# Performance work log

Hardware: AMD Instinct MI355X
Metric: run time of the kernel (lower is better)

## Reference

```python
import jax, jax.numpy as jnp
import numpy as np

OS_FACTOR = 1.5

def setup_inputs() -> dict:
    key = jax.random.key(0)
    k = jax.random.split(key, 5)
    B, T, I, H = 64, 1024, 1024, 1024
    s = 1.0 / np.sqrt(H).astype(np.float32)
    return {
        "x": jax.random.normal(k[0], (B, T, I), dtype=jnp.float32),
        "W_ih": jax.random.normal(k[1], (H, I), dtype=jnp.float32) * s,
        "W_hh": jax.random.normal(k[2], (H, H), dtype=jnp.float32) * s,
        "b_ih": jax.random.normal(k[3], (H,), dtype=jnp.float32) * s,
        "b_hh": jax.random.normal(k[4], (H,), dtype=jnp.float32) * s,
    }

def reference(x, W_ih, W_hh, b_ih, b_hh):
    B, T, I = x.shape
    H = W_hh.shape[0]
    delay_near = int(np.floor(OS_FACTOR))   # 1
    delay_far = int(np.ceil(OS_FACTOR))     # 2
    alpha = jnp.float32(OS_FACTOR - delay_near)  # 0.5
    # Precompute input projection for all steps (same math, batched GEMM): [T,B,H]
    xw = jnp.einsum('bti,hi->tbh', x, W_ih) + b_ih + b_hh
    # Circular delay buffer of the last `delay_far` states, zero-initialized.
    # In the torch code, negative indices into the zero `states` buffer read zeros,
    # which matches a zero-initialized buffer here.
    buf0 = jnp.zeros((delay_far, B, H), dtype=x.dtype)

    def step(buf, xw_t):
        # buf[-1] = state at t-1, buf[0] = state at t-delay_far
        h_read = (1.0 - alpha) * buf[delay_far - delay_near] + alpha * buf[0]
        h = jnp.tanh(xw_t + h_read @ W_hh.T)
        buf = jnp.concatenate([buf[1:], h[None]], axis=0)
        return buf, h

    _, states = jax.lax.scan(step, buf0, xw)   # states: [T,B,H]
    states = jnp.swapaxes(states, 0, 1)        # [B,T,H]
    h_final = states[:, -1, :][None]           # [1,B,H]
    return states, h_final
```

## Files before the change

### kernel.cpp

```cpp
#include <hip/hip_runtime.h>
#include <stdint.h>
#include <stddef.h>

#define TT 1024
#define BB 64
#define HH 1024
#define II 1024

typedef __attribute__((ext_vector_type(8))) short s16x8;
typedef __attribute__((ext_vector_type(4))) float f32x4;
typedef __attribute__((ext_vector_type(2))) unsigned u32x2;

#define WS_FLAGS 512
#define WS_RING  4096

static __device__ __forceinline__ unsigned short f2bf(float f) {
    union { float f; unsigned int u; } v; v.f = f;
    return (unsigned short)((v.u + 0x7fffu + ((v.u >> 16) & 1u)) >> 16);
}

static __device__ __forceinline__ s16x8 pack8(float4 a, float4 b) {
    s16x8 v;
    v[0] = (short)f2bf(a.x); v[1] = (short)f2bf(a.y);
    v[2] = (short)f2bf(a.z); v[3] = (short)f2bf(a.w);
    v[4] = (short)f2bf(b.x); v[5] = (short)f2bf(b.y);
    v[6] = (short)f2bf(b.z); v[7] = (short)f2bf(b.w);
    return v;
}

static __device__ __forceinline__ f32x4 zero4() {
    f32x4 v = {0.f, 0.f, 0.f, 0.f};
    return v;
}

static __device__ __forceinline__ s16x8 ld16_sc01(const void* p) {
    s16x8 v;
    asm volatile("global_load_dwordx4 %0, %1, off sc0 sc1" : "=v"(v) : "v"(p));
    return v;
}
static __device__ __forceinline__ unsigned ld4_sc01_wait(const void* p) {
    unsigned v;
    asm volatile("global_load_dword %0, %1, off sc0 sc1\n\ts_waitcnt vmcnt(0)"
                 : "=v"(v) : "v"(p) : "memory");
    return v;
}
static __device__ __forceinline__ void st8_sc01(void* p, u32x2 v) {
    asm volatile("global_store_dwordx2 %0, %1, off sc0 sc1" :: "v"(p), "v"(v) : "memory");
}
#define WAITV(n) do { asm volatile("s_waitcnt vmcnt(" #n ")" ::: "memory"); \
                      __builtin_amdgcn_sched_barrier(0); } while (0)

__global__ void init_ws(unsigned int* w) {
    for (int i = threadIdx.x; i < 640; i += 256)
        __hip_atomic_store(&w[i], 0u, __ATOMIC_RELAXED, __HIP_MEMORY_SCOPE_AGENT);
}

__global__ __launch_bounds__(256, 3) void xw_gemm(
    const float* __restrict__ X,
    const float* __restrict__ Wih,
    const float* __restrict__ bih,
    const float* __restrict__ bhh,
    float* __restrict__ out)
{
    __shared__ unsigned short As[128 * 64];
    __shared__ unsigned short Bs[128 * 64];

    const int tid  = threadIdx.x;
    const int lane = tid & 63;
    const int wid  = tid >> 6;
    const int bm = blockIdx.x >> 3;
    const int bn = blockIdx.x & 7;
    const size_t m0 = (size_t)bm * 128;
    const int n0 = bn * 128;
    const int wm = (wid >> 1) * 64;
    const int wn = (wid & 1) * 64;

    f32x4 acc[4][4];
#pragma unroll
    for (int i = 0; i < 4; ++i)
#pragma unroll
        for (int jj = 0; jj < 4; ++jj) acc[i][jj] = zero4();

    const int srow  = tid >> 1;
    const int shalf = tid & 1;
    const float* xp = X   + (m0 + srow) * (size_t)II + shalf * 32;
    const float* wp = Wih + (size_t)(n0 + srow) * II + shalf * 32;

    for (int kt = 0; kt < II / 64; ++kt) {
#pragma unroll
        for (int i = 0; i < 4; ++i) {
            float4 a0 = *(const float4*)(xp + i * 8);
            float4 a1 = *(const float4*)(xp + i * 8 + 4);
            float4 b0 = *(const float4*)(wp + i * 8);
            float4 b1 = *(const float4*)(wp + i * 8 + 4);
            const int c = shalf * 4 + i;
            const int cw = (c ^ (srow & 7)) << 3;
            *(s16x8*)&As[srow * 64 + cw] = pack8(a0, a1);
            *(s16x8*)&Bs[srow * 64 + cw] = pack8(b0, b1);
        }
        __syncthreads();

#pragma unroll
        for (int kk = 0; kk < 2; ++kk) {
            s16x8 af[4], bf[4];
            const int cs = kk * 4 + (lane >> 4);
#pragma unroll
            for (int mi = 0; mi < 4; ++mi) {
                const int r = wm + mi * 16 + (lane & 15);
                af[mi] = *(const s16x8*)&As[r * 64 + ((cs ^ (r & 7)) << 3)];
            }
#pragma unroll
            for (int ni = 0; ni < 4; ++ni) {
                const int r = wn + ni * 16 + (lane & 15);
                bf[ni] = *(const s16x8*)&Bs[r * 64 + ((cs ^ (r & 7)) << 3)];
            }
#pragma unroll
            for (int mi = 0; mi < 4; ++mi)
#pragma unroll
                for (int ni = 0; ni < 4; ++ni)
                    acc[mi][ni] = __builtin_amdgcn_mfma_f32_16x16x32_bf16(
                        af[mi], bf[ni], acc[mi][ni], 0, 0, 0);
        }
        __syncthreads();
        xp += 64; wp += 64;
    }

#pragma unroll
    for (int ni = 0; ni < 4; ++ni) {
        const int col = n0 + wn + ni * 16 + (lane & 15);
        const float bias = bih[col] + bhh[col];
#pragma unroll
        for (int mi = 0; mi < 4; ++mi) {
            const size_t row = m0 + wm + mi * 16 + ((lane >> 4) << 2);
#pragma unroll
            for (int r = 0; r < 4; ++r)
                out[(row + r) * (size_t)HH + col] = acc[mi][ni][r] + bias;
        }
    }
}

__global__ __launch_bounds__(256, 1) void rnn_scan(
    const float* __restrict__ Whh,
    float* __restrict__ out,
    void* __restrict__ ws)
{
    __shared__ unsigned short Hl[8 * 1024];

    const int tid  = threadIdx.x;
    const int lane = tid & 63;
    const int wid  = tid >> 6;
    const int g  = blockIdx.x >> 4;
    const int sl = blockIdx.x & 15;

    const int jb = sl * 64 + wid * 16;
    const int kg = lane >> 4;

    s16x8 afr[32];
    {
        const float* wr = Whh + (size_t)(jb + (lane & 15)) * HH + kg * 8;
#pragma unroll
        for (int c = 0; c < 32; ++c) {
            float4 p0 = *(const float4*)(wr + c * 32);
            float4 p1 = *(const float4*)(wr + c * 32 + 4);
            afr[c] = pack8(p0, p1);
        }
    }

    unsigned* fl = (unsigned*)((char*)ws + WS_FLAGS) + g * 64;
    char* rg = (char*)ws + WS_RING + (size_t)g * 32768;

    const int srow = tid >> 5;
    const int sseg = tid & 31;
    const char* sbase0 = rg + srow * 2048 + sseg * 16;
    const char* sbase1 = sbase0 + 16384;

    const int bl   = lane & 15;
    const int blv  = bl & 7;
    const int act  = bl < 8;
    const int b    = g * 8 + blv;
    const int f0   = jb + kg * 4;
    const int hrow = blv;

    float hprev[4];

    {
        const size_t idx = ((size_t)b * TT) * HH + f0;
        float4 xw4 = *(const float4*)(out + idx);
        float4 st;
        st.x = tanhf(xw4.x); st.y = tanhf(xw4.y);
        st.z = tanhf(xw4.z); st.w = tanhf(xw4.w);
        hprev[0] = st.x; hprev[1] = st.y; hprev[2] = st.z; hprev[3] = st.w;
        if (act) {
            *(float4*)(out + idx) = st;
            u32x2 pk;
            pk[0] = (unsigned)f2bf(0.5f * st.x) | ((unsigned)f2bf(0.5f * st.y) << 16);
            pk[1] = (unsigned)f2bf(0.5f * st.z) | ((unsigned)f2bf(0.5f * st.w) << 16);
            st8_sc01(rg + 16384 + blv * 2048 + f0 * 2, pk);
        }
    }
    asm volatile("s_waitcnt vmcnt(0)" ::: "memory");
    __syncthreads();
    if (tid == 0)
        __hip_atomic_store(&fl[sl], 1u, __ATOMIC_RELAXED, __HIP_MEMORY_SCOPE_AGENT);

#pragma unroll 1
    for (int t = 1; t < TT; ++t) {
        const size_t xidx = ((size_t)b * TT + t) * HH + f0;
        float4 xw4 = *(const float4*)(out + xidx);

        {
            const unsigned* myp = fl + (lane & 15);
            for (;;) {
                unsigned v = ld4_sc01_wait(myp);
                if (__all((int)(v >= (unsigned)t))) break;
                __builtin_amdgcn_s_sleep(1);
            }
            asm volatile("" ::: "memory");
            __builtin_amdgcn_sched_barrier(0);
        }

        {
            const char* sp = (t & 1) ? sbase1 : sbase0;
            s16x8 v[4];
#pragma unroll
            for (int i = 0; i < 4; ++i) v[i] = ld16_sc01(sp + i * 512);
#pragma unroll
            for (int i = 0; i < 4; ++i) {
                if (i == 0)      { WAITV(3); }
                else if (i == 1) { WAITV(2); }
                else if (i == 2) { WAITV(1); }
                else             { WAITV(0); }
                const int c = sseg + i * 32;
                *(s16x8*)&Hl[srow * 1024 + ((c ^ (srow & 7)) << 3)] = v[i];
            }
        }
        __syncthreads();

        f32x4 acc[4];
#pragma unroll
        for (int i = 0; i < 4; ++i) acc[i] = zero4();
#pragma unroll
        for (int kb = 0; kb < 4; ++kb) {
            s16x8 h8[8];
#pragma unroll
            for (int ki = 0; ki < 8; ++ki) {
                const int cs = (kb * 8 + ki) * 4 + kg;
                h8[ki] = *(const s16x8*)&Hl[hrow * 1024 + ((cs ^ (hrow & 7)) << 3)];
            }
#pragma unroll
            for (int ki = 0; ki < 8; ++ki)
                acc[ki & 3] = __builtin_amdgcn_mfma_f32_16x16x32_bf16(
                    afr[kb * 8 + ki], h8[ki], acc[ki & 3], 0, 0, 0);
        }
        f32x4 accT = acc[0] + acc[1] + acc[2] + acc[3];

        {
            float hn[4];
#pragma unroll
            for (int r = 0; r < 4; ++r)
                hn[r] = tanhf(accT[r] + ((const float*)&xw4)[r]);
            if (act) {
                float4 st; st.x = hn[0]; st.y = hn[1]; st.z = hn[2]; st.w = hn[3];
                *(float4*)(out + xidx) = st;
                if (t == TT - 1) {
                    *(float4*)(out + (size_t)BB * TT * HH + (size_t)b * HH + f0) = st;
                } else {
                    u32x2 pk;
                    pk[0] = (unsigned)f2bf(0.5f * (hn[0] + hprev[0])) |
                            ((unsigned)f2bf(0.5f * (hn[1] + hprev[1])) << 16);
                    pk[1] = (unsigned)f2bf(0.5f * (hn[2] + hprev[2])) |
                            ((unsigned)f2bf(0.5f * (hn[3] + hprev[3])) << 16);
                    char* rw = rg + (size_t)((t + 1) & 1) * 16384;
                    st8_sc01(rw + blv * 2048 + f0 * 2, pk);
                }
            }
#pragma unroll
            for (int r = 0; r < 4; ++r) hprev[r] = hn[r];
        }
        if (t < TT - 1) {
            asm volatile("s_waitcnt vmcnt(0)" ::: "memory");
            __syncthreads();
            if (tid == 0)
                __hip_atomic_store(&fl[sl], (unsigned)(t + 1),
                                   __ATOMIC_RELAXED, __HIP_MEMORY_SCOPE_AGENT);
        }
    }
}

extern "C" void kernel_launch(void* const* d_in, const int* in_sizes, int n_in,
                              void* d_out, int out_size, void* d_ws, size_t ws_size,
                              hipStream_t stream)
{
    const float* X   = (const float*)d_in[0];
    const float* Wih = (const float*)d_in[1];
    const float* Whh = (const float*)d_in[2];
    const float* bih = (const float*)d_in[3];
    const float* bhh = (const float*)d_in[4];
    float* out = (float*)d_out;

    init_ws<<<dim3(1), dim3(256), 0, stream>>>((unsigned int*)d_ws);
    xw_gemm<<<dim3(4096), dim3(256), 0, stream>>>(X, Wih, bih, bhh, out);
    rnn_scan<<<dim3(128), dim3(256), 0, stream>>>(Whh, out, d_ws);
}
```

Baseline: 3.600 ms.

## Halve scan workgroups, widen to 512 threads, and move state stores off the flag path

The recurrent scan now runs 8 workgroups of 512 threads per batch group instead of 16 of 256, so each step waits on half as many cross-workgroup flags. Each wave polls a single flag without sleeping, and the shared-state staging load is remapped to two 16-byte loads per thread. The fp32 state store to the output is moved after the flag publish so it leaves the critical path. The input-projection GEMM also gets a swizzled block order for better cache locality. The cost is more register pressure per workgroup and busier spin-polling.

After: 3.988 ms. 1.11x slower.

```diff
diff --git a/kernel.cpp b/kernel.cpp
--- a/kernel.cpp
+++ b/kernel.cpp
@@ -68,8 +68,9 @@
     const int tid  = threadIdx.x;
     const int lane = tid & 63;
     const int wid  = tid >> 6;
-    const int bm = blockIdx.x >> 3;
-    const int bn = blockIdx.x & 7;
+    const int L  = blockIdx.x;
+    const int bm = (L & 7) * 64 + (L >> 6);
+    const int bn = (L >> 3) & 7;
     const size_t m0 = (size_t)bm * 128;
     const int n0 = bn * 128;
     const int wm = (wid >> 1) * 64;
@@ -139,7 +140,7 @@
     }
 }
 
-__global__ __launch_bounds__(256, 1) void rnn_scan(
+__global__ __launch_bounds__(512, 1) void rnn_scan(
     const float* __restrict__ Whh,
     float* __restrict__ out,
     void* __restrict__ ws)
@@ -149,10 +150,10 @@
     const int tid  = threadIdx.x;
     const int lane = tid & 63;
     const int wid  = tid >> 6;
-    const int g  = blockIdx.x >> 4;
-    const int sl = blockIdx.x & 15;
-
-    const int jb = sl * 64 + wid * 16;
+    const int g  = blockIdx.x >> 3;
+    const int sl = blockIdx.x & 7;
+
+    const int jb = sl * 128 + wid * 16;
     const int kg = lane >> 4;
 
     s16x8 afr[32];
@@ -167,12 +168,13 @@
     }
 
     unsigned* fl = (unsigned*)((char*)ws + WS_FLAGS) + g * 64;
+    unsigned* myflag = fl + sl;
     char* rg = (char*)ws + WS_RING + (size_t)g * 32768;
 
-    const int srow = tid >> 5;
-    const int sseg = tid & 31;
-    const char* sbase0 = rg + srow * 2048 + sseg * 16;
+    const int strow = lane >> 3;
+    const char* sbase0 = rg + strow * 2048 + wid * 256 + (lane & 7) * 32;
     const char* sbase1 = sbase0 + 16384;
+    const int c0 = wid * 16 + (lane & 7) * 2;
 
     const int bl   = lane & 15;
     const int blv  = bl & 7;
@@ -191,17 +193,18 @@
         st.z = tanhf(xw4.z); st.w = tanhf(xw4.w);
         hprev[0] = st.x; hprev[1] = st.y; hprev[2] = st.z; hprev[3] = st.w;
         if (act) {
-            *(float4*)(out + idx) = st;
             u32x2 pk;
             pk[0] = (unsigned)f2bf(0.5f * st.x) | ((unsigned)f2bf(0.5f * st.y) << 16);
             pk[1] = (unsigned)f2bf(0.5f * st.z) | ((unsigned)f2bf(0.5f * st.w) << 16);
             st8_sc01(rg + 16384 + blv * 2048 + f0 * 2, pk);
         }
-    }
-    asm volatile("s_waitcnt vmcnt(0)" ::: "memory");
-    __syncthreads();
-    if (tid == 0)
-        __hip_atomic_store(&fl[sl], 1u, __ATOMIC_RELAXED, __HIP_MEMORY_SCOPE_AGENT);
+        asm volatile("s_waitcnt vmcnt(0)" ::: "memory");
+        __syncthreads();
+        if (tid == 0)
+            __hip_atomic_store(myflag, 1u, __ATOMIC_RELAXED,
+                               __HIP_MEMORY_SCOPE_AGENT);
+        if (act) *(float4*)(out + idx) = st;
+    }
 
 #pragma unroll 1
     for (int t = 1; t < TT; ++t) {
@@ -209,30 +212,18 @@
         float4 xw4 = *(const float4*)(out + xidx);
 
         {
-            const unsigned* myp = fl + (lane & 15);
             for (;;) {
-                unsigned v = ld4_sc01_wait(myp);
-                if (__all((int)(v >= (unsigned)t))) break;
-                __builtin_amdgcn_s_sleep(1);
-            }
-            asm volatile("" ::: "memory");
+                unsigned v = ld4_sc01_wait(fl + wid);
+                if (v >= (unsigned)t) break;
+            }
             __builtin_amdgcn_sched_barrier(0);
-        }
-
-        {
             const char* sp = (t & 1) ? sbase1 : sbase0;
-            s16x8 v[4];
-#pragma unroll
-            for (int i = 0; i < 4; ++i) v[i] = ld16_sc01(sp + i * 512);
-#pragma unroll
-            for (int i = 0; i < 4; ++i) {
-                if (i == 0)      { WAITV(3); }
-                else if (i == 1) { WAITV(2); }
-                else if (i == 2) { WAITV(1); }
-                else             { WAITV(0); }
-                const int c = sseg + i * 32;
-                *(s16x8*)&Hl[srow * 1024 + ((c ^ (srow & 7)) << 3)] = v[i];
-            }
+            s16x8 v0 = ld16_sc01(sp);
+            s16x8 v1 = ld16_sc01(sp + 16);
+            WAITV(1);
+            *(s16x8*)&Hl[strow * 1024 + ((c0 ^ (strow & 7)) << 3)] = v0;
+            WAITV(0);
+            *(s16x8*)&Hl[strow * 1024 + (((c0 + 1) ^ (strow & 7)) << 3)] = v1;
         }
         __syncthreads();
 
@@ -259,12 +250,9 @@
 #pragma unroll
             for (int r = 0; r < 4; ++r)
                 hn[r] = tanhf(accT[r] + ((const float*)&xw4)[r]);
-            if (act) {
-                float4 st; st.x = hn[0]; st.y = hn[1]; st.z = hn[2]; st.w = hn[3];
-                *(float4*)(out + xidx) = st;
-                if (t == TT - 1) {
-                    *(float4*)(out + (size_t)BB * TT * HH + (size_t)b * HH + f0) = st;
-                } else {
+            float4 st; st.x = hn[0]; st.y = hn[1]; st.z = hn[2]; st.w = hn[3];
+            if (t < TT - 1) {
+                if (act) {
                     u32x2 pk;
                     pk[0] = (unsigned)f2bf(0.5f * (hn[0] + hprev[0])) |
                             ((unsigned)f2bf(0.5f * (hn[1] + hprev[1])) << 16);
@@ -273,16 +261,20 @@
                     char* rw = rg + (size_t)((t + 1) & 1) * 16384;
                     st8_sc01(rw + blv * 2048 + f0 * 2, pk);
                 }
+                asm volatile("s_waitcnt vmcnt(0)" ::: "memory");
+                __syncthreads();
+                if (tid == 0)
+                    __hip_atomic_store(myflag, (unsigned)(t + 1),
+                                       __ATOMIC_RELAXED, __HIP_MEMORY_SCOPE_AGENT);
+                if (act) *(float4*)(out + xidx) = st;
+            } else {
+                if (act) {
+                    *(float4*)(out + xidx) = st;
+                    *(float4*)(out + (size_t)BB * TT * HH + (size_t)b * HH + f0) = st;
+                }
             }
 #pragma unroll
             for (int r = 0; r < 4; ++r) hprev[r] = hn[r];
-        }
-        if (t < TT - 1) {
-            asm volatile("s_waitcnt vmcnt(0)" ::: "memory");
-            __syncthreads();
-            if (tid == 0)
-                __hip_atomic_store(&fl[sl], (unsigned)(t + 1),
-                                   __ATOMIC_RELAXED, __HIP_MEMORY_SCOPE_AGENT);
         }
     }
 }
@@ -300,5 +292,5 @@
 
     init_ws<<<dim3(1), dim3(256), 0, stream>>>((unsigned int*)d_ws);
     xw_gemm<<<dim3(4096), dim3(256), 0, stream>>>(X, Wih, bih, bhh, out);
-    rnn_scan<<<dim3(128), dim3(256), 0, stream>>>(Whh, out, d_ws);
-}
+    rnn_scan<<<dim3(64), dim3(512), 0, stream>>>(Whh, out, d_ws);
+}
```
